# Optimization experiments

Measured on AMD Instinct MI355X. Metric: run time of the kernel, lower is better.

Reference implementation:

```python
import jax, jax.numpy as jnp
import numpy as np

T, B, D = 2048, 32, 1024
AH, H = 128, 8
N, N2 = D // H, AH // H


def setup_inputs() -> dict:
    key = jax.random.key(0)
    ks = jax.random.split(key, 7)
    s1 = 1.0 / np.sqrt(N)
    s2 = 1.0 / np.sqrt(N2)
    return {
        "hyp": jax.random.normal(ks[0], (T, B, D), dtype=jnp.float32),
        "W_w": jax.random.uniform(ks[1], (N2, N), jnp.float32, -s1, s1),
        "W_b": jax.random.uniform(ks[2], (N2,), jnp.float32, -s1, s1),
        "Wm_w": jax.random.uniform(ks[3], (N2, N), jnp.float32, -s1, s1),
        "Wm_b": jax.random.uniform(ks[4], (N2,), jnp.float32, -s1, s1),
        "Wh_w": jax.random.uniform(ks[5], (1, N2), jnp.float32, -s2, s2),
        "Wh_b": jax.random.uniform(ks[6], (1,), jnp.float32, -s2, s2),
        "dan_hidden_size": D,
        "attention_hidden_size": AH,
        "multihead_size": H,
    }


def reference(hyp, W_w, W_b, Wm_w, Wm_b, Wh_w, Wh_b,
              dan_hidden_size, attention_hidden_size, multihead_size):
    t, b, d = hyp.shape
    h_ = multihead_size
    n = d // h_
    # (T,B,D) -> (B,H,T,N); weights are shared across heads in the original loop
    x = jnp.transpose(hyp.reshape(t, b, h_, n), (1, 2, 0, 3))
    m = x.mean(axis=2, keepdims=True)                      # (B,H,1,N) mean over time
    gate_x = jnp.tanh(jnp.einsum('bhtn,kn->bhtk', x, W_w) + W_b)
    gate_m = jnp.tanh(jnp.einsum('bhtn,kn->bhtk', m, Wm_w) + Wm_b)
    hgate = gate_x * gate_m                                 # (B,H,T,N2)
    logits = jnp.einsum('bhtk,ok->bhto', hgate, Wh_w) + Wh_b  # (B,H,T,1)
    a = jax.nn.softmax(logits, axis=2)                      # softmax over time
    c = jnp.sum(a * x, axis=2)                              # (B,H,N)
    return c.reshape(b, h_ * n)
```

## Files before the change

### kernel.cpp

```cpp
#include <hip/hip_runtime.h>
#include <hip/hip_fp16.h>
#include <math.h>

#define T_   2048
#define B_   32
#define D_   1024
#define H_   8
#define N_   128
#define NK   16
#define TSPL 8
#define TBLK (T_/TSPL)
#define BD4  (B_*D_/4)
#define APS  132
#define LOG2E 1.4426950408889634f

typedef __attribute__((ext_vector_type(8))) short short8;
typedef __attribute__((ext_vector_type(4))) float f32x4;

__device__ __forceinline__ void split_bf16(float4 a, float4 b,
                                           short8& hi, short8& lo) {
    union { uint32_t u[4]; short8 v; } H, L;
    uint32_t x0 = __float_as_uint(a.x), x1 = __float_as_uint(a.y);
    uint32_t x2 = __float_as_uint(a.z), x3 = __float_as_uint(a.w);
    uint32_t x4 = __float_as_uint(b.x), x5 = __float_as_uint(b.y);
    uint32_t x6 = __float_as_uint(b.z), x7 = __float_as_uint(b.w);
    H.u[0] = (x0 >> 16) | (x1 & 0xFFFF0000u);
    H.u[1] = (x2 >> 16) | (x3 & 0xFFFF0000u);
    H.u[2] = (x4 >> 16) | (x5 & 0xFFFF0000u);
    H.u[3] = (x6 >> 16) | (x7 & 0xFFFF0000u);
    float l0 = a.x - __uint_as_float(x0 & 0xFFFF0000u);
    float l1 = a.y - __uint_as_float(x1 & 0xFFFF0000u);
    float l2 = a.z - __uint_as_float(x2 & 0xFFFF0000u);
    float l3 = a.w - __uint_as_float(x3 & 0xFFFF0000u);
    float l4 = b.x - __uint_as_float(x4 & 0xFFFF0000u);
    float l5 = b.y - __uint_as_float(x5 & 0xFFFF0000u);
    float l6 = b.z - __uint_as_float(x6 & 0xFFFF0000u);
    float l7 = b.w - __uint_as_float(x7 & 0xFFFF0000u);
    L.u[0] = (__float_as_uint(l0) >> 16) | (__float_as_uint(l1) & 0xFFFF0000u);
    L.u[1] = (__float_as_uint(l2) >> 16) | (__float_as_uint(l3) & 0xFFFF0000u);
    L.u[2] = (__float_as_uint(l4) >> 16) | (__float_as_uint(l5) & 0xFFFF0000u);
    L.u[3] = (__float_as_uint(l6) >> 16) | (__float_as_uint(l7) & 0xFFFF0000u);
    hi = H.v; lo = L.v;
}

__device__ __forceinline__ float tanh_fast(float d) {
    return 1.f - 2.f * __frcp_rn(exp2f(d * (2.f * LOG2E)) + 1.f);
}

#define LOADX(dst, step_) { \
    const int trow_ = t0 + (step_) * 64 + w * 16 + kk; \
    const size_t rb_ = (size_t)trow_ * BD4 + base4; \
    (dst)[0] = hyp4[rb_ + g * 2];      (dst)[1] = hyp4[rb_ + g * 2 + 1]; \
    (dst)[2] = hyp4[rb_ + 8 + g * 2];  (dst)[3] = hyp4[rb_ + 8 + g * 2 + 1]; \
    (dst)[4] = hyp4[rb_ + 16 + g * 2]; (dst)[5] = hyp4[rb_ + 16 + g * 2 + 1]; \
    (dst)[6] = hyp4[rb_ + 24 + g * 2]; (dst)[7] = hyp4[rb_ + 24 + g * 2 + 1]; }

__global__ __launch_bounds__(256, 4) void k_p(const float* __restrict__ hyp,
                                              const float* __restrict__ Ww,
                                              const float* __restrict__ Wb,
                                              float* __restrict__ part,
                                              __half* __restrict__ Pbuf) {
    __shared__ float red[4 * N_];
    const int tid  = threadIdx.x;
    const int lane = tid & 63;
    const int w    = tid >> 6;
    const int blk  = blockIdx.x;
    const int bh   = blk >> 3;
    const int spl  = blk & 7;
    const int b = bh >> 3, h = bh & 7;
    const int t0 = spl * TBLK;
    const float4* hyp4 = (const float4*)hyp;
    const float4* Ww4  = (const float4*)Ww;
    const int base4 = b * (D_ / 4) + h * (N_ / 4);
    const int kk = lane & 15;
    const int g  = lane >> 4;

    short8 wh[4], wlo[4];
#pragma unroll
    for (int ks = 0; ks < 4; ++ks) {
        float4 wa  = Ww4[kk * 32 + ks * 8 + g * 2];
        float4 wb4 = Ww4[kk * 32 + ks * 8 + g * 2 + 1];
        split_bf16(wa, wb4, wh[ks], wlo[ks]);
    }
    const float wbr = Wb[kk];

    float4 cs[8];
#pragma unroll
    for (int m = 0; m < 8; ++m) cs[m] = make_float4(0.f, 0.f, 0.f, 0.f);

#pragma unroll
    for (int step = 0; step < 4; ++step) {
        float4 xq[8];
        LOADX(xq, step);
#pragma unroll
        for (int m = 0; m < 8; ++m) {
            cs[m].x += xq[m].x; cs[m].y += xq[m].y;
            cs[m].z += xq[m].z; cs[m].w += xq[m].w;
        }
        f32x4 acc = {0.f, 0.f, 0.f, 0.f};
#pragma unroll
        for (int ks = 0; ks < 4; ++ks) {
            short8 xh, xl;
            split_bf16(xq[2*ks], xq[2*ks+1], xh, xl);
            acc = __builtin_amdgcn_mfma_f32_16x16x32_bf16(xh, wh[ks],  acc, 0, 0, 0);
            acc = __builtin_amdgcn_mfma_f32_16x16x32_bf16(xl, wh[ks],  acc, 0, 0, 0);
            acc = __builtin_amdgcn_mfma_f32_16x16x32_bf16(xh, wlo[ks], acc, 0, 0, 0);
        }
        const int tl = t0 + step * 64 + w * 16 + g * 4;
        const size_t pb = ((size_t)bh * T_ + tl) * NK + kk;
#pragma unroll
        for (int i = 0; i < 4; ++i)
            Pbuf[pb + (size_t)i * NK] = __float2half(tanh_fast(acc[i] + wbr));
    }
#pragma unroll
    for (int m = 0; m < 8; ++m) {
#pragma unroll
        for (int mask = 1; mask <= 8; mask <<= 1) {
            cs[m].x += __shfl_xor(cs[m].x, mask, 64);
            cs[m].y += __shfl_xor(cs[m].y, mask, 64);
            cs[m].z += __shfl_xor(cs[m].z, mask, 64);
            cs[m].w += __shfl_xor(cs[m].w, mask, 64);
        }
    }
    if (kk == 0) {
#pragma unroll
        for (int m = 0; m < 8; ++m) {
            int nb = 32 * (m >> 1) + 8 * g + 4 * (m & 1);
            red[w * N_ + nb + 0] = cs[m].x;
            red[w * N_ + nb + 1] = cs[m].y;
            red[w * N_ + nb + 2] = cs[m].z;
            red[w * N_ + nb + 3] = cs[m].w;
        }
    }
    __syncthreads();
    if (tid < N_)
        part[blk * N_ + tid] = (red[tid] + red[N_ + tid])
                             + (red[2*N_ + tid] + red[3*N_ + tid]);
}

__global__ __launch_bounds__(256, 4) void k_att(const float* __restrict__ hyp,
                                                const float* __restrict__ part,
                                                const float* __restrict__ Wmw,
                                                const float* __restrict__ Wmb,
                                                const float* __restrict__ Whw,
                                                const __half* __restrict__ Pbuf,
                                                float* __restrict__ attp) {
    __shared__ float red[4 * N_];
    __shared__ float zred[4];
    __shared__ float m_l[N_];
    __shared__ float gw_l[NK];
    const int tid  = threadIdx.x;
    const int lane = tid & 63;
    const int w    = tid >> 6;
    const int blk  = (B_ * H_ * TSPL - 1) - (int)blockIdx.x;
    const int bh   = blk >> 3;
    const int spl  = blk & 7;
    const int b = bh >> 3, h = bh & 7;
    const int t0 = spl * TBLK;
    const float4* hyp4 = (const float4*)hyp;
    const int base4 = b * (D_ / 4) + h * (N_ / 4);
    const int kk = lane & 15;
    const int g  = lane >> 4;

    if (tid < N_) {
        float s = 0.f;
#pragma unroll
        for (int s8 = 0; s8 < TSPL; ++s8) s += part[(bh * TSPL + s8) * N_ + tid];
        m_l[tid] = s * (1.f / (float)T_);
    }
    __syncthreads();
    if (tid < N_) {
        int k = tid >> 3, g3 = tid & 7;
        float dsum = 0.f;
#pragma unroll
        for (int i = 0; i < 16; ++i) {
            int n = g3 * 16 + i;
            dsum = fmaf(m_l[n], Wmw[k * N_ + n], dsum);
        }
        dsum += __shfl_xor(dsum, 1, 64);
        dsum += __shfl_xor(dsum, 2, 64);
        dsum += __shfl_xor(dsum, 4, 64);
        if (g3 == 0) gw_l[k] = tanhf(dsum + Wmb[k]) * Whw[k];
    }
    __syncthreads();
    float gmv[NK];
#pragma unroll
    for (int j = 0; j < NK; ++j) gmv[j] = gw_l[j];

    float4 cacc[8];
#pragma unroll
    for (int m = 0; m < 8; ++m) cacc[m] = make_float4(0.f, 0.f, 0.f, 0.f);
    float zacc = 0.f;

#pragma unroll
    for (int step = 0; step < 4; ++step) {
        const int tr = t0 + step * 64 + w * 16 + kk;
        union { uint4 u; __half2 h[8]; } P0, P1;
        const uint4* pv = (const uint4*)(Pbuf + (size_t)(bh * T_ + tr) * NK);
        P0.u = pv[0]; P1.u = pv[1];
        float4 xq[8];
        LOADX(xq, step);
        float lg = 0.f;
#pragma unroll
        for (int q = 0; q < 4; ++q) {
            float2 f0 = __half22float2(P0.h[q]);
            float2 f1 = __half22float2(P1.h[q]);
            lg = fmaf(f0.x, gmv[2*q + 0], lg);
            lg = fmaf(f0.y, gmv[2*q + 1], lg);
            lg = fmaf(f1.x, gmv[8 + 2*q + 0], lg);
            lg = fmaf(f1.y, gmv[8 + 2*q + 1], lg);
        }
        float e = exp2f(lg * LOG2E);
        zacc += e;
#pragma unroll
        for (int m = 0; m < 8; ++m) {
            cacc[m].x = fmaf(e, xq[m].x, cacc[m].x);
            cacc[m].y = fmaf(e, xq[m].y, cacc[m].y);
            cacc[m].z = fmaf(e, xq[m].z, cacc[m].z);
            cacc[m].w = fmaf(e, xq[m].w, cacc[m].w);
        }
    }
#pragma unroll
    for (int m = 0; m < 8; ++m) {
#pragma unroll
        for (int mask = 1; mask <= 8; mask <<= 1) {
            cacc[m].x += __shfl_xor(cacc[m].x, mask, 64);
            cacc[m].y += __shfl_xor(cacc[m].y, mask, 64);
            cacc[m].z += __shfl_xor(cacc[m].z, mask, 64);
            cacc[m].w += __shfl_xor(cacc[m].w, mask, 64);
        }
    }
    float z = zacc;
    z += __shfl_xor(z, 1, 64);
    z += __shfl_xor(z, 2, 64);
    z += __shfl_xor(z, 4, 64);
    z += __shfl_xor(z, 8, 64);
    if (kk == 0) {
#pragma unroll
        for (int m = 0; m < 8; ++m) {
            int nb = 32 * (m >> 1) + 8 * g + 4 * (m & 1);
            red[w * N_ + nb + 0] = cacc[m].x;
            red[w * N_ + nb + 1] = cacc[m].y;
            red[w * N_ + nb + 2] = cacc[m].z;
            red[w * N_ + nb + 3] = cacc[m].w;
        }
    }
    if (lane == 0) zred[w] = z;
    __syncthreads();
    if (tid < N_) {
        attp[(size_t)blk * APS + tid] =
            (red[tid] + red[N_ + tid]) + (red[2*N_ + tid] + red[3*N_ + tid]);
    } else if (tid == N_) {
        attp[(size_t)blk * APS + N_] =
            (zred[0] + zred[1]) + (zred[2] + zred[3]);
    }
}

__global__ __launch_bounds__(128) void k_red(const float* __restrict__ attp,
                                             float* __restrict__ out) {
    int bh = blockIdx.x, tid = threadIdx.x;
    float Z = 0.f, c = 0.f;
#pragma unroll
    for (int s = 0; s < TSPL; ++s) {
        const float* pp = &attp[(size_t)(bh * TSPL + s) * APS];
        Z += pp[N_];
        c += pp[tid];
    }
    out[bh * N_ + tid] = c / Z;
}

extern "C" void kernel_launch(void* const* d_in, const int* in_sizes, int n_in,
                              void* d_out, int out_size, void* d_ws, size_t ws_size,
                              hipStream_t stream) {
    const float* hyp = (const float*)d_in[0];
    const float* Ww  = (const float*)d_in[1];
    const float* Wb  = (const float*)d_in[2];
    const float* Wmw = (const float*)d_in[3];
    const float* Wmb = (const float*)d_in[4];
    const float* Whw = (const float*)d_in[5];
    float* out  = (float*)d_out;
    float* part = (float*)d_ws;
    float* attp = part + 2048 * N_;
    __half* Pbuf = (__half*)((char*)d_ws + (4 << 20));

    k_p  <<<dim3(B_ * H_ * TSPL), 256, 0, stream>>>(hyp, Ww, Wb, part, Pbuf);
    k_att<<<dim3(B_ * H_ * TSPL), 256, 0, stream>>>(hyp, part, Wmw, Wmb, Whw,
                                                    Pbuf, attp);
    k_red<<<dim3(B_ * H_), 128, 0, stream>>>(attp, out);
}
```

Baseline: 106.1 us.

## Recompute gate projection in attention kernel instead of storing fp16 P buffer

The first kernel becomes a pure time-sum pass with coalesced float4 loads. The MFMA gate projection and tanh move into the attention kernel, where each wave computes per-row logits directly with a cross-lane reduction and broadcast. This removes the fp16 intermediate buffer write and read (32 MB round trip). The price is doing the MFMA split-bf16 work in the second pass, which also reads hyp. The first pass now does only cheap loads and adds, so it should stay near bandwidth limits.

```diff
diff --git a/kernel.cpp b/kernel.cpp
--- a/kernel.cpp
+++ b/kernel.cpp
@@ -1,5 +1,4 @@
 #include <hip/hip_runtime.h>
-#include <hip/hip_fp16.h>
 #include <math.h>
 
 #define T_   2048
@@ -55,95 +54,55 @@
     (dst)[4] = hyp4[rb_ + 16 + g * 2]; (dst)[5] = hyp4[rb_ + 16 + g * 2 + 1]; \
     (dst)[6] = hyp4[rb_ + 24 + g * 2]; (dst)[7] = hyp4[rb_ + 24 + g * 2 + 1]; }
 
-__global__ __launch_bounds__(256, 4) void k_p(const float* __restrict__ hyp,
-                                              const float* __restrict__ Ww,
-                                              const float* __restrict__ Wb,
-                                              float* __restrict__ part,
-                                              __half* __restrict__ Pbuf) {
-    __shared__ float red[4 * N_];
-    const int tid  = threadIdx.x;
-    const int lane = tid & 63;
-    const int w    = tid >> 6;
-    const int blk  = blockIdx.x;
-    const int bh   = blk >> 3;
-    const int spl  = blk & 7;
+__global__ __launch_bounds__(256, 4) void k_mean(const float4* __restrict__ hyp4,
+                                                 float4* __restrict__ part4) {
+    __shared__ float4 red[8 * 32];
+    const int u = blockIdx.x;
+    const int bh = u >> 3, spl = u & 7;
     const int b = bh >> 3, h = bh & 7;
     const int t0 = spl * TBLK;
-    const float4* hyp4 = (const float4*)hyp;
-    const float4* Ww4  = (const float4*)Ww;
     const int base4 = b * (D_ / 4) + h * (N_ / 4);
-    const int kk = lane & 15;
-    const int g  = lane >> 4;
-
-    short8 wh[4], wlo[4];
-#pragma unroll
-    for (int ks = 0; ks < 4; ++ks) {
-        float4 wa  = Ww4[kk * 32 + ks * 8 + g * 2];
-        float4 wb4 = Ww4[kk * 32 + ks * 8 + g * 2 + 1];
-        split_bf16(wa, wb4, wh[ks], wlo[ks]);
-    }
-    const float wbr = Wb[kk];
-
-    float4 cs[8];
-#pragma unroll
-    for (int m = 0; m < 8; ++m) cs[m] = make_float4(0.f, 0.f, 0.f, 0.f);
-
-#pragma unroll
-    for (int step = 0; step < 4; ++step) {
-        float4 xq[8];
-        LOADX(xq, step);
-#pragma unroll
-        for (int m = 0; m < 8; ++m) {
-            cs[m].x += xq[m].x; cs[m].y += xq[m].y;
-            cs[m].z += xq[m].z; cs[m].w += xq[m].w;
-        }
-        f32x4 acc = {0.f, 0.f, 0.f, 0.f};
-#pragma unroll
-        for (int ks = 0; ks < 4; ++ks) {
-            short8 xh, xl;
-            split_bf16(xq[2*ks], xq[2*ks+1], xh, xl);
-            acc = __builtin_amdgcn_mfma_f32_16x16x32_bf16(xh, wh[ks],  acc, 0, 0, 0);
-            acc = __builtin_amdgcn_mfma_f32_16x16x32_bf16(xl, wh[ks],  acc, 0, 0, 0);
-            acc = __builtin_amdgcn_mfma_f32_16x16x32_bf16(xh, wlo[ks], acc, 0, 0, 0);
-        }
-        const int tl = t0 + step * 64 + w * 16 + g * 4;
-        const size_t pb = ((size_t)bh * T_ + tl) * NK + kk;
-#pragma unroll
-        for (int i = 0; i < 4; ++i)
-            Pbuf[pb + (size_t)i * NK] = __float2half(tanh_fast(acc[i] + wbr));
-    }
-#pragma unroll
-    for (int m = 0; m < 8; ++m) {
-#pragma unroll
-        for (int mask = 1; mask <= 8; mask <<= 1) {
-            cs[m].x += __shfl_xor(cs[m].x, mask, 64);
-            cs[m].y += __shfl_xor(cs[m].y, mask, 64);
-            cs[m].z += __shfl_xor(cs[m].z, mask, 64);
-            cs[m].w += __shfl_xor(cs[m].w, mask, 64);
-        }
-    }
-    if (kk == 0) {
-#pragma unroll
-        for (int m = 0; m < 8; ++m) {
-            int nb = 32 * (m >> 1) + 8 * g + 4 * (m & 1);
-            red[w * N_ + nb + 0] = cs[m].x;
-            red[w * N_ + nb + 1] = cs[m].y;
-            red[w * N_ + nb + 2] = cs[m].z;
-            red[w * N_ + nb + 3] = cs[m].w;
-        }
-    }
-    __syncthreads();
-    if (tid < N_)
-        part[blk * N_ + tid] = (red[tid] + red[N_ + tid])
-                             + (red[2*N_ + tid] + red[3*N_ + tid]);
+    const int col4 = threadIdx.x & 31;
+    const int tg   = threadIdx.x >> 5;
+    const size_t cbase = (size_t)(t0 + tg * 32) * BD4 + base4 + col4;
+
+    float4 a0 = {0,0,0,0}, a1 = {0,0,0,0}, a2 = {0,0,0,0}, a3 = {0,0,0,0};
+#pragma unroll
+    for (int i = 0; i < 32; i += 4) {
+        float4 v0 = hyp4[cbase + (size_t)(i+0) * BD4];
+        float4 v1 = hyp4[cbase + (size_t)(i+1) * BD4];
+        float4 v2 = hyp4[cbase + (size_t)(i+2) * BD4];
+        float4 v3 = hyp4[cbase + (size_t)(i+3) * BD4];
+        a0.x += v0.x; a0.y += v0.y; a0.z += v0.z; a0.w += v0.w;
+        a1.x += v1.x; a1.y += v1.y; a1.z += v1.z; a1.w += v1.w;
+        a2.x += v2.x; a2.y += v2.y; a2.z += v2.z; a2.w += v2.w;
+        a3.x += v3.x; a3.y += v3.y; a3.z += v3.z; a3.w += v3.w;
+    }
+    float4 s;
+    s.x = (a0.x + a1.x) + (a2.x + a3.x);
+    s.y = (a0.y + a1.y) + (a2.y + a3.y);
+    s.z = (a0.z + a1.z) + (a2.z + a3.z);
+    s.w = (a0.w + a1.w) + (a2.w + a3.w);
+    red[tg * 32 + col4] = s;
+    __syncthreads();
+    if (threadIdx.x < 32) {
+        float4 t = {0,0,0,0};
+#pragma unroll
+        for (int gg = 0; gg < 8; ++gg) {
+            float4 v = red[gg * 32 + threadIdx.x];
+            t.x += v.x; t.y += v.y; t.z += v.z; t.w += v.w;
+        }
+        part4[(size_t)u * 32 + threadIdx.x] = t;
+    }
 }
 
 __global__ __launch_bounds__(256, 4) void k_att(const float* __restrict__ hyp,
+                                                const float* __restrict__ Ww,
+                                                const float* __restrict__ Wb,
                                                 const float* __restrict__ part,
                                                 const float* __restrict__ Wmw,
                                                 const float* __restrict__ Wmb,
                                                 const float* __restrict__ Whw,
-                                                const __half* __restrict__ Pbuf,
                                                 float* __restrict__ attp) {
     __shared__ float red[4 * N_];
     __shared__ float zred[4];
@@ -158,6 +117,7 @@
     const int b = bh >> 3, h = bh & 7;
     const int t0 = spl * TBLK;
     const float4* hyp4 = (const float4*)hyp;
+    const float4* Ww4  = (const float4*)Ww;
     const int base4 = b * (D_ / 4) + h * (N_ / 4);
     const int kk = lane & 15;
     const int g  = lane >> 4;
@@ -183,9 +143,16 @@
         if (g3 == 0) gw_l[k] = tanhf(dsum + Wmb[k]) * Whw[k];
     }
     __syncthreads();
-    float gmv[NK];
-#pragma unroll
-    for (int j = 0; j < NK; ++j) gmv[j] = gw_l[j];
+
+    short8 wh[4], wlo[4];
+#pragma unroll
+    for (int ks = 0; ks < 4; ++ks) {
+        float4 wa  = Ww4[kk * 32 + ks * 8 + g * 2];
+        float4 wb4 = Ww4[kk * 32 + ks * 8 + g * 2 + 1];
+        split_bf16(wa, wb4, wh[ks], wlo[ks]);
+    }
+    const float wbr  = Wb[kk];
+    const float gmwr = gw_l[kk];
 
     float4 cacc[8];
 #pragma unroll
@@ -194,30 +161,41 @@
 
 #pragma unroll
     for (int step = 0; step < 4; ++step) {
-        const int tr = t0 + step * 64 + w * 16 + kk;
-        union { uint4 u; __half2 h[8]; } P0, P1;
-        const uint4* pv = (const uint4*)(Pbuf + (size_t)(bh * T_ + tr) * NK);
-        P0.u = pv[0]; P1.u = pv[1];
         float4 xq[8];
         LOADX(xq, step);
-        float lg = 0.f;
-#pragma unroll
-        for (int q = 0; q < 4; ++q) {
-            float2 f0 = __half22float2(P0.h[q]);
-            float2 f1 = __half22float2(P1.h[q]);
-            lg = fmaf(f0.x, gmv[2*q + 0], lg);
-            lg = fmaf(f0.y, gmv[2*q + 1], lg);
-            lg = fmaf(f1.x, gmv[8 + 2*q + 0], lg);
-            lg = fmaf(f1.y, gmv[8 + 2*q + 1], lg);
-        }
-        float e = exp2f(lg * LOG2E);
-        zacc += e;
+        f32x4 acc = {0.f, 0.f, 0.f, 0.f};
+#pragma unroll
+        for (int ks = 0; ks < 4; ++ks) {
+            short8 xh, xl;
+            split_bf16(xq[2*ks], xq[2*ks+1], xh, xl);
+            acc = __builtin_amdgcn_mfma_f32_16x16x32_bf16(xh, wh[ks],  acc, 0, 0, 0);
+            acc = __builtin_amdgcn_mfma_f32_16x16x32_bf16(xl, wh[ks],  acc, 0, 0, 0);
+            acc = __builtin_amdgcn_mfma_f32_16x16x32_bf16(xh, wlo[ks], acc, 0, 0, 0);
+        }
+        float pl[4];
+#pragma unroll
+        for (int i = 0; i < 4; ++i)
+            pl[i] = tanh_fast(acc[i] + wbr) * gmwr;
+#pragma unroll
+        for (int i = 0; i < 4; ++i) {
+            pl[i] += __shfl_xor(pl[i], 1, 64);
+            pl[i] += __shfl_xor(pl[i], 2, 64);
+            pl[i] += __shfl_xor(pl[i], 4, 64);
+            pl[i] += __shfl_xor(pl[i], 8, 64);
+        }
+        float e0 = exp2f(pl[0] * LOG2E), e1 = exp2f(pl[1] * LOG2E);
+        float e2 = exp2f(pl[2] * LOG2E), e3 = exp2f(pl[3] * LOG2E);
+        zacc += (e0 + e1) + (e2 + e3);
+        int src = (kk >> 2) << 4;
+        float s0 = __shfl(e0, src, 64), s1 = __shfl(e1, src, 64);
+        float s2 = __shfl(e2, src, 64), s3 = __shfl(e3, src, 64);
+        float E = (kk & 2) ? ((kk & 1) ? s3 : s2) : ((kk & 1) ? s1 : s0);
 #pragma unroll
         for (int m = 0; m < 8; ++m) {
-            cacc[m].x = fmaf(e, xq[m].x, cacc[m].x);
-            cacc[m].y = fmaf(e, xq[m].y, cacc[m].y);
-            cacc[m].z = fmaf(e, xq[m].z, cacc[m].z);
-            cacc[m].w = fmaf(e, xq[m].w, cacc[m].w);
+            cacc[m].x = fmaf(E, xq[m].x, cacc[m].x);
+            cacc[m].y = fmaf(E, xq[m].y, cacc[m].y);
+            cacc[m].z = fmaf(E, xq[m].z, cacc[m].z);
+            cacc[m].w = fmaf(E, xq[m].w, cacc[m].w);
         }
     }
 #pragma unroll
@@ -231,10 +209,8 @@
         }
     }
     float z = zacc;
-    z += __shfl_xor(z, 1, 64);
-    z += __shfl_xor(z, 2, 64);
-    z += __shfl_xor(z, 4, 64);
-    z += __shfl_xor(z, 8, 64);
+    z += __shfl_xor(z, 16, 64);
+    z += __shfl_xor(z, 32, 64);
     if (kk == 0) {
 #pragma unroll
         for (int m = 0; m < 8; ++m) {
@@ -281,10 +257,10 @@
     float* out  = (float*)d_out;
     float* part = (float*)d_ws;
     float* attp = part + 2048 * N_;
-    __half* Pbuf = (__half*)((char*)d_ws + (4 << 20));
-
-    k_p  <<<dim3(B_ * H_ * TSPL), 256, 0, stream>>>(hyp, Ww, Wb, part, Pbuf);
-    k_att<<<dim3(B_ * H_ * TSPL), 256, 0, stream>>>(hyp, part, Wmw, Wmb, Whw,
-                                                    Pbuf, attp);
-    k_red<<<dim3(B_ * H_), 128, 0, stream>>>(attp, out);
-}
+
+    k_mean<<<dim3(B_ * H_ * TSPL), 256, 0, stream>>>((const float4*)hyp,
+                                                     (float4*)part);
+    k_att <<<dim3(B_ * H_ * TSPL), 256, 0, stream>>>(hyp, Ww, Wb, part,
+                                                     Wmw, Wmb, Whw, attp);
+    k_red <<<dim3(B_ * H_), 128, 0, stream>>>(attp, out);
+}
```

After: 163.1 us. 1.54x slower.
